# Performance work log

Hardware: AMD Instinct MI355X
Metric: run time of the kernel (lower is better)

## Reference

```python
import jax, jax.numpy as jnp
import numpy as np

# Mamba2 defaults: d_model=256, d_state=64, d_conv=4, expand=2, headdim=64, ngroups=1
D_MODEL = 256
NB = 2            # num_blocks
D_STATE = 64
D_CONV = 4
D_INNER = 2 * D_MODEL          # 512
HEADDIM = 64
NHEADS = D_INNER // HEADDIM    # 8
CONV_DIM = D_INNER + 2 * D_STATE           # 640
D_IN_PROJ = 2 * D_INNER + 2 * D_STATE + NHEADS  # 1160
EPS = 1e-5


def setup_inputs() -> dict:
    key = jax.random.key(0)
    ks = jax.random.split(key, 10)
    x = jax.random.normal(ks[0], (8, 32, 32, D_MODEL), dtype=jnp.float32)
    in_proj_w = jax.random.normal(ks[1], (NB, D_IN_PROJ, D_MODEL), dtype=jnp.float32) * 0.02
    conv_w = jax.random.normal(ks[2], (NB, CONV_DIM, 1, D_CONV), dtype=jnp.float32) * 0.2
    conv_b = jax.random.normal(ks[3], (NB, CONV_DIM), dtype=jnp.float32) * 0.02
    dt_bias = jax.random.normal(ks[4], (NB, NHEADS), dtype=jnp.float32) * 0.5
    # A_log = log(A), A ~ U[1,16) as in mamba2 init
    A_log = jnp.log(jax.random.uniform(ks[5], (NB, NHEADS), minval=1.0, maxval=16.0, dtype=jnp.float32))
    D = jax.random.normal(ks[6], (NB, NHEADS), dtype=jnp.float32) * 0.1 + 1.0
    norm_w = jnp.ones((NB, D_INNER), dtype=jnp.float32)
    out_proj_w = jax.random.normal(ks[7], (NB, D_MODEL, D_INNER), dtype=jnp.float32) * 0.02
    return {"x": x, "in_proj_w": in_proj_w, "conv_w": conv_w, "conv_b": conv_b,
            "dt_bias": dt_bias, "A_log": A_log, "D": D, "norm_w": norm_w,
            "out_proj_w": out_proj_w}


def _mamba2_block(h, wi, cw, cb, dtb, a_log, d_skip, nw, wo):
    B, L, _ = h.shape
    zxbcdt = jnp.einsum('blc,pc->blp', h, wi)                 # (B,L,1160)
    z = zxbcdt[..., :D_INNER]                                 # (B,L,512)
    xBC = zxbcdt[..., D_INNER:D_INNER + CONV_DIM]             # (B,L,640)
    dt = jax.nn.softplus(zxbcdt[..., -NHEADS:] + dtb)         # (B,L,8)

    # causal depthwise conv1d, kernel 4, left pad 3
    xBC = jax.lax.conv_general_dilated(
        xBC.swapaxes(1, 2), cw, window_strides=(1,), padding=[(D_CONV - 1, 0)],
        dimension_numbers=('NCH', 'OIH', 'NCH'), feature_group_count=CONV_DIM)
    xBC = jax.nn.silu((xBC + cb[None, :, None]).swapaxes(1, 2))  # (B,L,640)

    xs = xBC[..., :D_INNER].reshape(B, L, NHEADS, HEADDIM)    # (B,L,h,p)
    Bm = xBC[..., D_INNER:D_INNER + D_STATE]                  # (B,L,s) ngroups=1
    Cm = xBC[..., D_INNER + D_STATE:]                         # (B,L,s)

    A = -jnp.exp(a_log)                                       # (h,)
    dA = jnp.exp(dt * A)                                      # (B,L,h)

    def step(s, inp):
        dA_t, dt_t, x_t, B_t, C_t = inp  # (B,h),(B,h),(B,h,p),(B,s),(B,s)
        s = s * dA_t[:, :, None, None] + (dt_t[:, :, None] * x_t)[..., None] * B_t[:, None, None, :]
        y = jnp.einsum('bhps,bs->bhp', s, C_t)
        return s, y

    s0 = jnp.zeros((B, NHEADS, HEADDIM, D_STATE), dtype=h.dtype)
    _, ys = jax.lax.scan(step, s0, (dA.swapaxes(0, 1), dt.swapaxes(0, 1),
                                    xs.swapaxes(0, 1), Bm.swapaxes(0, 1), Cm.swapaxes(0, 1)))
    y = ys.swapaxes(0, 1) + d_skip[:, None] * xs              # (B,L,h,p)
    y = y.reshape(B, L, D_INNER) * jax.nn.silu(z)             # gate
    y = y * jax.lax.rsqrt(jnp.mean(y * y, axis=-1, keepdims=True) + EPS) * nw  # gated RMSNorm
    return jnp.einsum('bld,cd->blc', y, wo)


def reference(x, in_proj_w, conv_w, conv_b, dt_bias, A_log, D, norm_w, out_proj_w):
    B, H, W, C = x.shape
    h = x.reshape(B, H * W, C)
    for i in range(NB):  # stacked blocks; Dropout is identity at inference
        h = _mamba2_block(h, in_proj_w[i], conv_w[i], conv_b[i], dt_bias[i],
                          A_log[i], D[i], norm_w[i], out_proj_w[i])
    return h.reshape(B, H, W, C)
```

## Files before the change

### kernel.cpp

```cpp
#include <hip/hip_runtime.h>
#include <hip/hip_bf16.h>
#include <math.h>

#define D_MODEL   256
#define D_STATE   64
#define D_CONV    4
#define D_INNER   512
#define HEADDIM   64
#define NHEADS    8
#define CONV_DIM  640
#define D_IN_PROJ 1160
#define ZXP       1280
#define SEQLEN    1024
#define BATCH     8
#define NROWS     8192
#define EPS       1e-5f
#define CHUNK     64
#define NCHUNK    (SEQLEN / CHUNK)

typedef __attribute__((ext_vector_type(8))) short bf16x8;
typedef __attribute__((ext_vector_type(4))) short s16x4;
typedef __attribute__((ext_vector_type(8))) unsigned short u16x8;
typedef __attribute__((ext_vector_type(4))) unsigned short u16x4;
typedef __attribute__((ext_vector_type(4))) float f32x4;
typedef unsigned int u32;
typedef unsigned short u16;

__device__ __forceinline__ void cp16(const short* g, short* l) {
    __builtin_amdgcn_global_load_lds((const __attribute__((address_space(1))) u32*)g,
                                     (__attribute__((address_space(3))) u32*)l, 16, 0, 0);
}
__device__ __forceinline__ u16 bfc(float f) {
    union { __hip_bfloat16 h; u16 u; } cv;
    cv.h = __float2bfloat16(f);
    return cv.u;
}
__device__ __forceinline__ float bf2f(u16 u) {
    union { u32 v; float f; } cv;
    cv.v = ((u32)u) << 16;
    return cv.f;
}
__device__ __forceinline__ float silu_f(float a) {
    return a * __builtin_amdgcn_rcpf(1.f + __expf(-a));
}
__device__ __forceinline__ void store_out(float* p, float v) { *p = v; }
__device__ __forceinline__ void store_out(__hip_bfloat16* p, float v) { *p = __float2bfloat16(v); }

__device__ __forceinline__ int swz(int row, int col) {
    return row * 64 + (((col & 56) ^ ((row & 7) << 3)) | (col & 7));
}
__device__ __forceinline__ bf16x8 ldfrag(const short* base, int row, int oct) {
    return *(const bf16x8*)&base[row * 64 + ((oct * 8) ^ ((row & 7) * 8))];
}
__device__ __forceinline__ void wr2u(short* base, int row, int col2, u16 a, u16 b) {
    int idx = row * 64 + (((col2 & 56) ^ ((row & 7) << 3)) | (col2 & 6));
    *(u32*)&base[idx] = (u32)a | ((u32)b << 16);
}

template <typename OUT, bool WITH_DT>
__global__ __launch_bounds__(256) void gemm_mfma(const short* __restrict__ A,
                                                 const short* __restrict__ W,
                                                 OUT* __restrict__ C,
                                                 float* __restrict__ dtout,
                                                 int N, int K, int lda) {
    __shared__ short As[128 * 32];
    __shared__ short Ws[128 * 32];
    const int tid  = threadIdx.x;
    const int m0   = blockIdx.y * 128;
    const int n0   = blockIdx.x * 128;
    const int wave = tid >> 6;
    const int lane = tid & 63;
    const int wm   = (wave & 1) * 64;
    const int wn   = (wave >> 1) * 64;
    const int lm   = lane & 15;
    const int lq   = lane >> 4;

    const int sr   = tid >> 2;
    const int soct = (tid & 3) ^ (sr & 3);
    const short* ga = A + (size_t)(m0 + sr) * lda + soct * 8;
    const short* gw = W + (size_t)(n0 + sr) * K + soct * 8;
    short* la = &As[tid * 8];
    short* lw = &Ws[tid * 8];
    const size_t ga2 = (size_t)64 * lda;
    const size_t gw2 = (size_t)64 * K;

    const int oa = (lq ^ (lm & 3)) * 8;

    f32x4 acc[4][4] = {};

    for (int k0 = 0; k0 < K; k0 += 32) {
        cp16(ga,       la);
        cp16(ga + ga2, la + 64 * 32);
        cp16(gw,       lw);
        cp16(gw + gw2, lw + 64 * 32);
        ga += 32; gw += 32;
        __syncthreads();
        bf16x8 af[4], bfr[4];
        #pragma unroll
        for (int i = 0; i < 4; i++) {
            af[i]  = *(const bf16x8*)&As[(wm + i * 16 + lm) * 32 + oa];
            bfr[i] = *(const bf16x8*)&Ws[(wn + i * 16 + lm) * 32 + oa];
        }
        #pragma unroll
        for (int i = 0; i < 4; i++)
            #pragma unroll
            for (int j = 0; j < 4; j++)
                acc[i][j] = __builtin_amdgcn_mfma_f32_16x16x32_bf16(af[i], bfr[j], acc[i][j], 0, 0, 0);
        __syncthreads();
    }
    #pragma unroll
    for (int i = 0; i < 4; i++)
        #pragma unroll
        for (int r = 0; r < 4; r++) {
            int m = m0 + wm + i * 16 + lq * 4 + r;
            #pragma unroll
            for (int j = 0; j < 4; j++) {
                int n = n0 + wn + j * 16 + lm;
                float v = acc[i][j][r];
                store_out(&C[(size_t)m * N + n], v);
                if (WITH_DT) {
                    if (n >= D_IN_PROJ - NHEADS && n < D_IN_PROJ)
                        dtout[(size_t)m * NHEADS + (n - (D_IN_PROJ - NHEADS))] = v;
                }
            }
        }
}

#define NX_C  (NROWS * D_MODEL)
#define NWI_C (2 * ZXP * D_MODEL)
#define NWO_C (2 * D_MODEL * D_INNER)
__global__ __launch_bounds__(256) void cast_all_kernel(
    const float* __restrict__ x, const float* __restrict__ wi,
    const float* __restrict__ wo,
    u16* __restrict__ xb, u16* __restrict__ wib, u16* __restrict__ wob)
{
    int idx = blockIdx.x * 256 + threadIdx.x;
    if (idx < NX_C) { xb[idx] = bfc(x[idx]); return; }
    idx -= NX_C;
    if (idx < NWI_C) {
        int k = idx & 255;
        int rb = idx >> 8;
        int r = rb % ZXP;
        int blk = rb / ZXP;
        float v = (r < D_IN_PROJ)
            ? wi[(size_t)blk * D_IN_PROJ * D_MODEL + (size_t)r * D_MODEL + k] : 0.f;
        wib[idx] = bfc(v);
        return;
    }
    idx -= NWI_C;
    wob[idx] = bfc(wo[idx]);
}

__global__ __launch_bounds__(256) void ssd_intra_kernel(
    const u16* __restrict__ zx,
    const float* __restrict__ dtbuf,
    const float* __restrict__ dt_bias, const float* __restrict__ A_log,
    const float* __restrict__ cw, const float* __restrict__ cb,
    const float* __restrict__ Dp,
    u16* __restrict__ ys, u16* __restrict__ Schunk,
    float* __restrict__ adec, u16* __restrict__ Cb)
{
    const int h   = blockIdx.x & 7;
    const int c   = (blockIdx.x >> 3) & 15;
    const int b   = blockIdx.x >> 7;
    const int tid = threadIdx.x;
    const int row0 = b * SEQLEN + c * CHUNK;

    __shared__ short Xt[64 * 64];
    __shared__ short Bn[64 * 64];
    __shared__ short Cn[64 * 64];
    __shared__ short BTw[64 * 64];
    __shared__ float cums[64], dts_s[64], ws_s[64];
    __shared__ float4 wls[192];
    __shared__ float  bls[192];

    if (tid < 64) {
        const float A = -__expf(A_log[h] * 1.44269504089f);
        float raw = dtbuf[(size_t)(row0 + tid) * NHEADS + h] + dt_bias[h];
        float dtv = (raw > 20.f) ? raw : log1pf(__expf(raw));
        float v = dtv * A;
        #pragma unroll
        for (int off = 1; off < 64; off <<= 1) {
            float o = __shfl_up(v, off, 64);
            if (tid >= off) v += o;
        }
        float tot = __shfl(v, 63, 64);
        cums[tid]  = v;
        dts_s[tid] = dtv;
        ws_s[tid]  = __expf(tot - v) * dtv;
        adec[(size_t)(b * NHEADS + h) * SEQLEN + c * CHUNK + tid] = __expf(v);
    } else {
        int wi = tid - 64;
        int g = wi >> 6, k = wi & 63;
        int ch = (g == 0) ? h * HEADDIM + k : (g == 1 ? 512 + k : 576 + k);
        wls[wi] = *(const float4*)&cw[ch * 4];
        bls[wi] = cb[ch];
    }
    __syncthreads();

    {
        const int t2 = (tid >> 3) * 2;
        const int c8 = (tid & 7) * 8;
        const int lb = c * CHUNK + t2;
        const u16* zb = zx + (size_t)(row0 + t2) * ZXP + D_INNER;
        const float w0 = ws_s[t2], w1 = ws_s[t2 + 1];
        u16x8 zz;
        #pragma unroll
        for (int q = 0; q < 8; q++) zz[q] = 0;

        #pragma unroll
        for (int g = 0; g < 3; g++) {
            const int gc = (g == 0) ? h * HEADDIM + c8 : (g == 1 ? 512 + c8 : 576 + c8);
            const u16* p = zb + gc;
            u16x8 r0 = (lb >= 3) ? *(const u16x8*)(p - 3 * ZXP) : zz;
            u16x8 r1 = (lb >= 2) ? *(const u16x8*)(p - 2 * ZXP) : zz;
            u16x8 r2 = (lb >= 1) ? *(const u16x8*)(p - 1 * ZXP) : zz;
            u16x8 r3 = *(const u16x8*)p;
            u16x8 r4 = *(const u16x8*)(p + ZXP);
            u16x8 o0, o1;
            #pragma unroll
            for (int k = 0; k < 8; k++) {
                float4 w4  = wls[g * 64 + c8 + k];
                float bias = bls[g * 64 + c8 + k];
                float a0 = bias, a1 = bias;
                a0 = fmaf(bf2f(r0[k]), w4.x, a0);
                a0 = fmaf(bf2f(r1[k]), w4.y, a0);
                a0 = fmaf(bf2f(r2[k]), w4.z, a0);
                a0 = fmaf(bf2f(r3[k]), w4.w, a0);
                a1 = fmaf(bf2f(r1[k]), w4.x, a1);
                a1 = fmaf(bf2f(r2[k]), w4.y, a1);
                a1 = fmaf(bf2f(r3[k]), w4.z, a1);
                a1 = fmaf(bf2f(r4[k]), w4.w, a1);
                float s0 = silu_f(a0);
                float s1 = silu_f(a1);
                if (g == 0) {
                    wr2u(Xt, c8 + k, t2, bfc(s0), bfc(s1));
                } else if (g == 1) {
                    o0[k] = bfc(s0); o1[k] = bfc(s1);
                    wr2u(BTw, c8 + k, t2, bfc(s0 * w0), bfc(s1 * w1));
                } else {
                    o0[k] = bfc(s0); o1[k] = bfc(s1);
                }
            }
            if (g == 1) {
                *(u16x8*)&Bn[swz(t2,     c8)] = o0;
                *(u16x8*)&Bn[swz(t2 + 1, c8)] = o1;
            } else if (g == 2) {
                *(u16x8*)&Cn[swz(t2,     c8)] = o0;
                *(u16x8*)&Cn[swz(t2 + 1, c8)] = o1;
                if (h == 0) {
                    *(u16x8*)&Cb[(size_t)(row0 + t2)     * 64 + c8] = o0;
                    *(u16x8*)&Cb[(size_t)(row0 + t2 + 1) * 64 + c8] = o1;
                }
            }
        }
    }
    __syncthreads();

    const int lane = tid & 63, w = tid >> 6;
    const int lm = lane & 15, lq = lane >> 4;
    const int tau0 = 16 * w + lq * 4;

    bf16x8 aG0 = ldfrag(Bn, 16 * w + lm, lq);
    bf16x8 aG1 = ldfrag(Bn, 16 * w + lm, 4 + lq);
    f32x4 g[4] = {};
    #pragma unroll
    for (int j = 0; j < 4; j++) {
        g[j] = __builtin_amdgcn_mfma_f32_16x16x32_bf16(aG0, ldfrag(Cn, 16 * j + lm, lq),     g[j], 0, 0, 0);
        g[j] = __builtin_amdgcn_mfma_f32_16x16x32_bf16(aG1, ldfrag(Cn, 16 * j + lm, 4 + lq), g[j], 0, 0, 0);
    }
    float ctau[4], dtau[4];
    *(float4*)&ctau[0] = *(const float4*)&cums[tau0];
    *(float4*)&dtau[0] = *(const float4*)&dts_s[tau0];
    s16x4 mp[4];
    #pragma unroll
    for (int j = 0; j < 4; j++) {
        int t = 16 * j + lm;
        float ct = cums[t];
        #pragma unroll
        for (int r = 0; r < 4; r++) {
            int tau = tau0 + r;
            float m = (t >= tau) ? g[j][r] * __expf(ct - ctau[r]) * dtau[r] : 0.f;
            mp[j][r] = (short)bfc(m);
        }
    }
    __syncthreads();
    #pragma unroll
    for (int j = 0; j < 4; j++)
        *(s16x4*)&Cn[swz(16 * j + lm, tau0)] = mp[j];
    __syncthreads();

    bf16x8 aY0 = ldfrag(Cn,  16 * w + lm, lq);
    bf16x8 aY1 = ldfrag(Cn,  16 * w + lm, 4 + lq);
    bf16x8 aS0 = ldfrag(BTw, 16 * w + lm, lq);
    bf16x8 aS1 = ldfrag(BTw, 16 * w + lm, 4 + lq);
    f32x4 yv[4] = {}, sv[4] = {};
    #pragma unroll
    for (int j = 0; j < 4; j++) {
        bf16x8 xf0 = ldfrag(Xt, 16 * j + lm, lq);
        bf16x8 xf1 = ldfrag(Xt, 16 * j + lm, 4 + lq);
        yv[j] = __builtin_amdgcn_mfma_f32_16x16x32_bf16(aY0, xf0, yv[j], 0, 0, 0);
        yv[j] = __builtin_amdgcn_mfma_f32_16x16x32_bf16(aY1, xf1, yv[j], 0, 0, 0);
        sv[j] = __builtin_amdgcn_mfma_f32_16x16x32_bf16(aS0, xf0, sv[j], 0, 0, 0);
        sv[j] = __builtin_amdgcn_mfma_f32_16x16x32_bf16(aS1, xf1, sv[j], 0, 0, 0);
    }
    const float Dh = Dp[h];
    const int mrow = 16 * w + lq * 4;
    #pragma unroll
    for (int j = 0; j < 4; j++)
        #pragma unroll
        for (int r = 0; r < 4; r++) {
            float xv = bf2f((u16)Xt[swz(16 * j + lm, mrow + r)]);
            ys[(size_t)(row0 + mrow + r) * D_INNER + h * HEADDIM + 16 * j + lm]
                = bfc(yv[j][r] + Dh * xv);
        }
    u16* sb = Schunk + (size_t)((b * NCHUNK + c) * NHEADS + h) * 4096;
    #pragma unroll
    for (int j = 0; j < 4; j++)
        #pragma unroll
        for (int r = 0; r < 4; r++)
            sb[(mrow + r) * 64 + 16 * j + lm] = bfc(sv[j][r]);
}

__global__ __launch_bounds__(256) void ssd_state_scan_kernel(
    u16* __restrict__ Schunk, const float* __restrict__ adec)
{
    const int q  = blockIdx.x & 3;
    const int bh = blockIdx.x >> 2;
    const int b  = bh >> 3, h = bh & 7;
    const int base = q * 1024 + threadIdx.x * 4;

    u16x4 v[NCHUNK];
    float atot[NCHUNK];
    #pragma unroll
    for (int c = 0; c < NCHUNK; c++) {
        v[c] = *(const u16x4*)&Schunk[(size_t)((b * NCHUNK + c) * NHEADS + h) * 4096 + base];
        atot[c] = adec[(size_t)bh * SEQLEN + c * CHUNK + 63];
    }
    float run[4] = {0.f, 0.f, 0.f, 0.f};
    #pragma unroll
    for (int c = 0; c < NCHUNK; c++) {
        u16x4 pv;
        #pragma unroll
        for (int k = 0; k < 4; k++) pv[k] = bfc(run[k]);
        *(u16x4*)&Schunk[(size_t)((b * NCHUNK + c) * NHEADS + h) * 4096 + base] = pv;
        #pragma unroll
        for (int k = 0; k < 4; k++)
            run[k] = fmaf(atot[c], run[k], bf2f(v[c][k]));
    }
}

template <typename OUT>
__global__ __launch_bounds__(512) void ssd_finish_proj_kernel(
    const u16* __restrict__ Cb, const u16* __restrict__ zx,
    const u16* __restrict__ ysin, const u16* __restrict__ Schunk,
    const float* __restrict__ adec, const float* __restrict__ nw,
    const u16* __restrict__ wo, OUT* __restrict__ Cout)
{
    const int half = blockIdx.x & 1;
    const int c    = (blockIdx.x >> 1) & 15;
    const int b    = blockIdx.x >> 5;
    const int tid  = threadIdx.x;
    const int row0 = b * SEQLEN + c * CHUNK + half * 32;

    __shared__ short y_lds[32 * 512];
    __shared__ short reg2[256 * 64];
    __shared__ float a_s[256];
    __shared__ float nw_s[512];
    __shared__ float ps[128];
    __shared__ float scl[32];

    short* Ct  = reg2;
    short* STs = reg2 + 32 * 64;
    short* Ws  = reg2;

    const int lane = tid & 63, w = tid >> 6;
    const int lm = lane & 15, lq = lane >> 4;
    const int rf  = w & 1;
    const int cf4 = w >> 1;

    nw_s[tid] = nw[tid];
    if (tid < 256) {
        int t2 = tid >> 3, n8 = (tid & 7) * 8;
        *(u16x8*)&Ct[swz(t2, n8)] = *(const u16x8*)&Cb[(size_t)(row0 + t2) * 64 + n8];
        a_s[tid] = adec[(size_t)(b * NHEADS + (tid >> 5)) * SEQLEN + c * CHUNK + half * 32 + (tid & 31)];
        const u16* sb = Schunk + (size_t)((b * NCHUNK + c) * NHEADS) * 4096;
        int n2 = (tid >> 3) * 2, p8 = (tid & 7) * 8;
        u16x8 s0 = *(const u16x8*)&sb[(size_t)n2 * 64 + p8];
        u16x8 s1 = *(const u16x8*)&sb[(size_t)(n2 + 1) * 64 + p8];
        #pragma unroll
        for (int k = 0; k < 8; k++)
            wr2u(STs, p8 + k, n2, s0[k], s1[k]);
    }
    __syncthreads();

    bf16x8 aC0 = ldfrag(Ct, 16 * rf + lm, lq);
    bf16x8 aC1 = ldfrag(Ct, 16 * rf + lm, 4 + lq);
    float ssloc[4] = {0.f, 0.f, 0.f, 0.f};

    for (int h = 0; h < 8; h++) {
        const int n = cf4 * 16 + lm;
        f32x4 U = {};
        U = __builtin_amdgcn_mfma_f32_16x16x32_bf16(aC0, ldfrag(STs, n, lq),     U, 0, 0, 0);
        U = __builtin_amdgcn_mfma_f32_16x16x32_bf16(aC1, ldfrag(STs, n, 4 + lq), U, 0, 0, 0);
        __syncthreads();
        if (h < 7 && tid < 256) {
            const u16* sb = Schunk + (size_t)((b * NCHUNK + c) * NHEADS + h + 1) * 4096;
            int n2 = (tid >> 3) * 2, p8 = (tid & 7) * 8;
            u16x8 s0 = *(const u16x8*)&sb[(size_t)n2 * 64 + p8];
            u16x8 s1 = *(const u16x8*)&sb[(size_t)(n2 + 1) * 64 + p8];
            #pragma unroll
            for (int k = 0; k < 8; k++)
                wr2u(STs, p8 + k, n2, s0[k], s1[k]);
        }
        {
            const int col = h * 64 + cf4 * 16 + lm;
            const float nwv = nw_s[col];
            #pragma unroll
            for (int r = 0; r < 4; r++) {
                int row = 16 * rf + lq * 4 + r;
                size_t grow = (size_t)(row0 + row);
                float u = U[r] * a_s[h * 32 + row] + bf2f(ysin[grow * D_INNER + col]);
                float zv = bf2f(zx[grow * ZXP + col]);
                float v = u * silu_f(zv);
                ssloc[r] = fmaf(v, v, ssloc[r]);
                y_lds[row * 512 + ((((col >> 3) ^ (row & 7)) << 3) | (col & 7))] = (short)bfc(v * nwv);
            }
        }
        __syncthreads();
    }

    #pragma unroll
    for (int r = 0; r < 4; r++) {
        float s = ssloc[r];
        s += __shfl_xor(s, 1, 64); s += __shfl_xor(s, 2, 64);
        s += __shfl_xor(s, 4, 64); s += __shfl_xor(s, 8, 64);
        if (lm == 0) ps[cf4 * 32 + 16 * rf + lq * 4 + r] = s;
    }
    __syncthreads();
    if (tid < 32)
        scl[tid] = rsqrtf((ps[tid] + ps[32 + tid] + ps[64 + tid] + ps[96 + tid])
                          * (1.f / (float)D_INNER) + EPS);
    __syncthreads();

    f32x4 acc[4] = {};
    const int arow = 16 * rf + lm;
    for (int kk = 0; kk < 8; kk++) {
        {
            int rr = tid >> 3;
            int oc = tid & 7;
            #pragma unroll
            for (int q = 0; q < 4; q++) {
                int row = rr + q * 64;
                const u16* src = wo + (size_t)row * 512 + kk * 64 + ((oc ^ (row & 7)) * 8);
                cp16((const short*)src, &Ws[q * 4096 + tid * 8]);
            }
        }
        __syncthreads();
        bf16x8 aY0 = *(const bf16x8*)&y_lds[arow * 512 + ((kk * 8) | (lq       ^ (arow & 7))) * 8];
        bf16x8 aY1 = *(const bf16x8*)&y_lds[arow * 512 + ((kk * 8) | ((4 + lq) ^ (arow & 7))) * 8];
        #pragma unroll
        for (int j = 0; j < 4; j++) {
            int n = cf4 * 64 + j * 16 + lm;
            acc[j] = __builtin_amdgcn_mfma_f32_16x16x32_bf16(aY0, ldfrag(Ws, n, lq),     acc[j], 0, 0, 0);
            acc[j] = __builtin_amdgcn_mfma_f32_16x16x32_bf16(aY1, ldfrag(Ws, n, 4 + lq), acc[j], 0, 0, 0);
        }
        __syncthreads();
    }
    const int mrow = 16 * rf + lq * 4;
    #pragma unroll
    for (int r = 0; r < 4; r++) {
        float scale = scl[mrow + r];
        size_t m = (size_t)(row0 + mrow + r);
        #pragma unroll
        for (int j = 0; j < 4; j++) {
            int n = cf4 * 64 + j * 16 + lm;
            store_out(&Cout[m * D_MODEL + n], acc[j][r] * scale);
        }
    }
}

extern "C" void kernel_launch(void* const* d_in, const int* in_sizes, int n_in,
                              void* d_out, int out_size, void* d_ws, size_t ws_size,
                              hipStream_t stream) {
    const float* x          = (const float*)d_in[0];
    const float* in_proj_w  = (const float*)d_in[1];
    const float* conv_w     = (const float*)d_in[2];
    const float* conv_b     = (const float*)d_in[3];
    const float* dt_bias    = (const float*)d_in[4];
    const float* A_log      = (const float*)d_in[5];
    const float* Dp         = (const float*)d_in[6];
    const float* norm_w     = (const float*)d_in[7];
    const float* out_proj_w = (const float*)d_in[8];
    float* out = (float*)d_out;

    u16*   buf_zx = (u16*)d_ws;
    u16*   buf_cb = buf_zx + (size_t)NROWS * ZXP;
    u16*   buf_ys = buf_cb + (size_t)NROWS * 64;
    u16*   buf_S  = buf_ys + (size_t)NROWS * D_INNER;
    u16*   buf_hb = buf_S  + (size_t)BATCH * NCHUNK * NHEADS * 4096;
    u16*   buf_wi = buf_hb + (size_t)NROWS * D_MODEL;
    u16*   buf_wo = buf_wi + (size_t)2 * ZXP * D_MODEL;
    float* buf_dt = (float*)(buf_wo + (size_t)2 * D_MODEL * D_INNER);
    float* buf_a  = buf_dt + (size_t)NROWS * NHEADS;

    cast_all_kernel<<<(NX_C + NWI_C + NWO_C) / 256, 256, 0, stream>>>(
        x, in_proj_w, out_proj_w, buf_hb, buf_wi, buf_wo);

    for (int i = 0; i < 2; i++) {
        gemm_mfma<__hip_bfloat16, true><<<dim3(ZXP / 128, NROWS / 128), 256, 0, stream>>>(
            (const short*)buf_hb, (const short*)(buf_wi + (size_t)i * ZXP * D_MODEL),
            (__hip_bfloat16*)buf_zx, buf_dt, ZXP, D_MODEL, D_MODEL);

        ssd_intra_kernel<<<BATCH * NCHUNK * NHEADS, 256, 0, stream>>>(
            buf_zx, buf_dt,
            dt_bias + i * NHEADS, A_log + i * NHEADS,
            conv_w + (size_t)i * CONV_DIM * D_CONV, conv_b + (size_t)i * CONV_DIM,
            Dp + i * NHEADS, buf_ys, buf_S, buf_a, buf_cb);

        ssd_state_scan_kernel<<<BATCH * NHEADS * 4, 256, 0, stream>>>(buf_S, buf_a);

        if (i == 0) {
            ssd_finish_proj_kernel<__hip_bfloat16><<<BATCH * NCHUNK * 2, 512, 0, stream>>>(
                buf_cb, buf_zx, buf_ys, buf_S, buf_a,
                norm_w, (const u16*)buf_wo, (__hip_bfloat16*)buf_hb);
        } else {
            ssd_finish_proj_kernel<float><<<BATCH * NCHUNK * 2, 512, 0, stream>>>(
                buf_cb, buf_zx, buf_ys, buf_S, buf_a,
                norm_w + D_INNER, (const u16*)(buf_wo + (size_t)D_MODEL * D_INNER), out);
        }
    }
}
```

Before: 178.3 us.

## Double-buffer state and out_proj weight tiles in SSD finish kernel

The ssd_finish_proj kernel now keeps two LDS buffers each for the per-head chunk states and the out_proj weight tiles. The next tile is loaded while MFMAs run on the current one, and the first weight tile is prefetched during the RMS reduction. This removes one barrier per iteration in both loops and hides global load latency. In exchange, LDS use rises to about 100KB per block, which may lower occupancy, and correctness depends on cp16 being synchronous or else fenced by the remaining barriers.

```diff
diff --git a/kernel.cpp b/kernel.cpp
--- a/kernel.cpp
+++ b/kernel.cpp
@@ -363,16 +363,18 @@
     const int tid  = threadIdx.x;
     const int row0 = b * SEQLEN + c * CHUNK + half * 32;
 
-    __shared__ short y_lds[32 * 512];
-    __shared__ short reg2[256 * 64];
-    __shared__ float a_s[256];
-    __shared__ float nw_s[512];
-    __shared__ float ps[128];
-    __shared__ float scl[32];
-
-    short* Ct  = reg2;
-    short* STs = reg2 + 32 * 64;
-    short* Ws  = reg2;
+    __shared__ __align__(16) short smem[51008];
+    short* y_lds = smem;
+    short* Ct    = smem + 16384;
+    short* STs0  = smem + 16384 + 2048;
+    short* STs1  = STs0 + 4096;
+    short* Ws0   = smem + 16384;
+    short* Ws1   = smem + 32768;
+    float* fb    = (float*)(smem + 49152);
+    float* a_s   = fb;
+    float* nw_s  = fb + 256;
+    float* ps    = fb + 768;
+    float* scl   = fb + 896;
 
     const int lane = tid & 63, w = tid >> 6;
     const int lm = lane & 15, lq = lane >> 4;
@@ -390,7 +392,7 @@
         u16x8 s1 = *(const u16x8*)&sb[(size_t)(n2 + 1) * 64 + p8];
         #pragma unroll
         for (int k = 0; k < 8; k++)
-            wr2u(STs, p8 + k, n2, s0[k], s1[k]);
+            wr2u(STs0, p8 + k, n2, s0[k], s1[k]);
     }
     __syncthreads();
 
@@ -399,11 +401,8 @@
     float ssloc[4] = {0.f, 0.f, 0.f, 0.f};
 
     for (int h = 0; h < 8; h++) {
-        const int n = cf4 * 16 + lm;
-        f32x4 U = {};
-        U = __builtin_amdgcn_mfma_f32_16x16x32_bf16(aC0, ldfrag(STs, n, lq),     U, 0, 0, 0);
-        U = __builtin_amdgcn_mfma_f32_16x16x32_bf16(aC1, ldfrag(STs, n, 4 + lq), U, 0, 0, 0);
-        __syncthreads();
+        short* Scur = (h & 1) ? STs1 : STs0;
+        short* Snxt = (h & 1) ? STs0 : STs1;
         if (h < 7 && tid < 256) {
             const u16* sb = Schunk + (size_t)((b * NCHUNK + c) * NHEADS + h + 1) * 4096;
             int n2 = (tid >> 3) * 2, p8 = (tid & 7) * 8;
@@ -411,8 +410,12 @@
             u16x8 s1 = *(const u16x8*)&sb[(size_t)(n2 + 1) * 64 + p8];
             #pragma unroll
             for (int k = 0; k < 8; k++)
-                wr2u(STs, p8 + k, n2, s0[k], s1[k]);
-        }
+                wr2u(Snxt, p8 + k, n2, s0[k], s1[k]);
+        }
+        const int n = cf4 * 16 + lm;
+        f32x4 U = {};
+        U = __builtin_amdgcn_mfma_f32_16x16x32_bf16(aC0, ldfrag(Scur, n, lq),     U, 0, 0, 0);
+        U = __builtin_amdgcn_mfma_f32_16x16x32_bf16(aC1, ldfrag(Scur, n, 4 + lq), U, 0, 0, 0);
         {
             const int col = h * 64 + cf4 * 16 + lm;
             const float nwv = nw_s[col];
@@ -430,6 +433,16 @@
         __syncthreads();
     }
 
+    {
+        int rr = tid >> 3, oc = tid & 7;
+        #pragma unroll
+        for (int q = 0; q < 4; q++) {
+            int row = rr + q * 64;
+            const u16* src = wo + (size_t)row * 512 + ((oc ^ (row & 7)) * 8);
+            cp16((const short*)src, &Ws0[q * 4096 + tid * 8]);
+        }
+    }
+
     #pragma unroll
     for (int r = 0; r < 4; r++) {
         float s = ssloc[r];
@@ -446,26 +459,26 @@
     f32x4 acc[4] = {};
     const int arow = 16 * rf + lm;
     for (int kk = 0; kk < 8; kk++) {
-        {
-            int rr = tid >> 3;
-            int oc = tid & 7;
+        short* Wcur = (kk & 1) ? Ws1 : Ws0;
+        short* Wnxt = (kk & 1) ? Ws0 : Ws1;
+        if (kk < 7) {
+            int rr = tid >> 3, oc = tid & 7;
             #pragma unroll
             for (int q = 0; q < 4; q++) {
                 int row = rr + q * 64;
-                const u16* src = wo + (size_t)row * 512 + kk * 64 + ((oc ^ (row & 7)) * 8);
-                cp16((const short*)src, &Ws[q * 4096 + tid * 8]);
+                const u16* src = wo + (size_t)row * 512 + (kk + 1) * 64 + ((oc ^ (row & 7)) * 8);
+                cp16((const short*)src, &Wnxt[q * 4096 + tid * 8]);
             }
         }
-        __syncthreads();
         bf16x8 aY0 = *(const bf16x8*)&y_lds[arow * 512 + ((kk * 8) | (lq       ^ (arow & 7))) * 8];
         bf16x8 aY1 = *(const bf16x8*)&y_lds[arow * 512 + ((kk * 8) | ((4 + lq) ^ (arow & 7))) * 8];
         #pragma unroll
         for (int j = 0; j < 4; j++) {
             int n = cf4 * 64 + j * 16 + lm;
-            acc[j] = __builtin_amdgcn_mfma_f32_16x16x32_bf16(aY0, ldfrag(Ws, n, lq),     acc[j], 0, 0, 0);
-            acc[j] = __builtin_amdgcn_mfma_f32_16x16x32_bf16(aY1, ldfrag(Ws, n, 4 + lq), acc[j], 0, 0, 0);
-        }
-        __syncthreads();
+            acc[j] = __builtin_amdgcn_mfma_f32_16x16x32_bf16(aY0, ldfrag(Wcur, n, lq),     acc[j], 0, 0, 0);
+            acc[j] = __builtin_amdgcn_mfma_f32_16x16x32_bf16(aY1, ldfrag(Wcur, n, 4 + lq), acc[j], 0, 0, 0);
+        }
+        if (kk < 7) __syncthreads();
     }
     const int mrow = 16 * rf + lq * 4;
     #pragma unroll
```

Result: faster. 174.2 us (-2.3%).
